# Optimization experiments

Hardware: AMD Instinct MI355X
Metric: run time of the kernel (lower is better)

The kernel has to match this reference:

```python
import jax, jax.numpy as jnp
import numpy as np
from jax import lax

T, B = 80, 32
ACT, CIN, HID, LSTM_H = 16, 4, 512, 256

def _conv(x, w, b, stride, pad):
    y = lax.conv_general_dilated(x, w, (stride, stride), [(pad, pad), (pad, pad)],
                                 dimension_numbers=('NCHW', 'OIHW', 'NCHW'))
    return y + b[None, :, None, None]

def setup_inputs() -> dict:
    key = jax.random.key(0)
    ks = jax.random.split(key, 20)
    s = 0.02
    return {
        'x': jax.random.uniform(ks[0], (T, B, CIN, 84, 84), dtype=jnp.float32),
        'last_action': jax.random.randint(ks[1], (T, B), 0, ACT),
        'reward': jax.random.normal(ks[2], (T, B), dtype=jnp.float32),
        'dones': jnp.zeros((T, B), dtype=bool),
        'hx': jax.random.normal(ks[3], (2, B, LSTM_H), dtype=jnp.float32) * s,
        'conv1_w': jax.random.normal(ks[4], (32, CIN, 8, 8), jnp.float32) * s,
        'conv1_b': jnp.zeros((32,), jnp.float32),
        'conv2_w': jax.random.normal(ks[5], (64, 32, 4, 4), jnp.float32) * s,
        'conv2_b': jnp.zeros((64,), jnp.float32),
        'conv3_w': jax.random.normal(ks[6], (64, 64, 3, 3), jnp.float32) * s,
        'conv3_b': jnp.zeros((64,), jnp.float32),
        'fc_w': jax.random.normal(ks[7], (HID, 3136), jnp.float32) * s,
        'fc_b': jnp.zeros((HID,), jnp.float32),
        'lstm_wih': jax.random.normal(ks[8], (4 * LSTM_H, HID + ACT + 1), jnp.float32) * s,
        'lstm_whh': jax.random.normal(ks[9], (4 * LSTM_H, LSTM_H), jnp.float32) * s,
        'lstm_bih': jnp.zeros((4 * LSTM_H,), jnp.float32),
        'lstm_bhh': jnp.zeros((4 * LSTM_H,), jnp.float32),
        'actor_w': jax.random.normal(ks[10], (ACT, LSTM_H), jnp.float32) * s,
        'actor_b': jnp.zeros((ACT,), jnp.float32),
        'critic_w': jax.random.normal(ks[11], (1, LSTM_H), jnp.float32) * s,
        'critic_b': jnp.zeros((1,), jnp.float32),
    }

def reference(x, last_action, reward, dones, hx,
              conv1_w, conv1_b, conv2_w, conv2_b, conv3_w, conv3_b,
              fc_w, fc_b, lstm_wih, lstm_whh, lstm_bih, lstm_bhh,
              actor_w, actor_b, critic_w, critic_b):
    seq_len, bs = x.shape[0], x.shape[1]
    xf = x.reshape(seq_len * bs, CIN, 84, 84)          # combine time & batch
    la = jax.nn.one_hot(last_action.reshape(-1), ACT, dtype=jnp.float32)
    rw = reward.reshape(-1, 1)

    lrelu = lambda v: jax.nn.leaky_relu(v, 0.01)
    h = lrelu(_conv(xf, conv1_w, conv1_b, 4, 1))       # [N,32,20,20]
    h = lrelu(_conv(h, conv2_w, conv2_b, 2, 0))        # [N,64,9,9]
    h = lrelu(_conv(h, conv3_w, conv3_b, 1, 0))        # [N,64,7,7]
    h = h.reshape(h.shape[0], -1)                      # [N,3136]
    h = lrelu(h @ fc_w.T + fc_b)                       # [N,512]
    h = jnp.concatenate([h, rw, la], axis=1)           # [N,529]
    h = h.reshape(seq_len, bs, -1)

    def step(carry, inp):
        xt, dt = inp                                   # [bs,529], [bs] bool
        carry = jnp.where(dt[None, :, None], 0.0, carry)
        hh, cc = carry[0], carry[1]
        gates = xt @ lstm_wih.T + lstm_bih + hh @ lstm_whh.T + lstm_bhh
        i, f, g, o = jnp.split(gates, 4, axis=1)
        cc = jax.nn.sigmoid(f) * cc + jax.nn.sigmoid(i) * jnp.tanh(g)
        hh = jax.nn.sigmoid(o) * jnp.tanh(cc)
        return jnp.stack([hh, cc], 0), hh

    _, hs = lax.scan(step, hx, (h, dones))             # hs: [T,bs,256]
    feat = hs.reshape(seq_len * bs, LSTM_H)

    logits = feat @ actor_w.T + actor_b                # [N,16]
    values = feat @ critic_w.T + critic_b              # [N,1]
    logits = jnp.where(jnp.isnan(logits), jnp.float32(1e-12), logits)
    return logits.reshape(seq_len, -1, bs), values.reshape(seq_len, bs)
```

## Files before the change

### kernel.cpp

```cpp
#include <hip/hip_runtime.h>
#include <math.h>

#define T_ 80
#define B_ 32
#define N_ 2560
#define LH_ 256

typedef __attribute__((ext_vector_type(8))) short short8;
typedef __attribute__((ext_vector_type(4))) float f32x4;
#define MFMA16(a, b, c) __builtin_amdgcn_mfma_f32_16x16x32_bf16((a), (b), (c), 0, 0, 0)

__device__ __forceinline__ float lrelu(float v) { return v > 0.f ? v : 0.01f * v; }
__device__ __forceinline__ short f2bf(float f) {
    unsigned u = __float_as_uint(f);
    return (short)((u + 0x7fffu + ((u >> 16) & 1u)) >> 16);
}

__global__ void pack_all_k(const float* __restrict__ c1w, const float* __restrict__ c2w,
                           const float* __restrict__ c3w, const float* __restrict__ fcw,
                           const float* __restrict__ wih,
                           short* __restrict__ wp1, short* __restrict__ wp2,
                           short* __restrict__ wp3, short* __restrict__ wfcP,
                           short* __restrict__ wihP) {
    __shared__ short rowb[3136];
    int blk = blockIdx.x, tidx = threadIdx.x;
    if (blk < 512) {
        int j = blk;
        for (int i = tidx; i < 3136; i += 256) rowb[i] = f2bf(fcw[j * 3136 + i]);
        __syncthreads();
        for (int i = tidx; i < 3136; i += 256) {
            int p = i >> 6, oc = i & 63;
            wfcP[j * 3136 + i] = rowb[oc * 49 + p];
        }
        return;
    }
    blk -= 512;
    if (blk < 2048) {
        int g = blk * 256 + tidx;
        int r = g >> 9, k = g & 511;
        wihP[g] = f2bf(wih[r * 529 + k]);
        return;
    }
    blk -= 2048;
    if (blk < 32) {
        int g = blk * 256 + tidx;
        int ky = g >> 10, oc = (g >> 5) & 31, k = g & 31, kx = k >> 2, ci = k & 3;
        wp1[g] = f2bf(c1w[((oc * 4 + ci) * 8 + ky) * 8 + kx]);
        return;
    }
    blk -= 32;
    if (blk < 128) {
        int g = blk * 256 + tidx;
        int t = g >> 11, oc = (g >> 5) & 63, ci = g & 31, ky = t >> 2, kx = t & 3;
        wp2[g] = f2bf(c2w[((oc * 32 + ci) * 4 + ky) * 4 + kx]);
        return;
    }
    blk -= 128;
    {
        int g = blk * 256 + tidx;
        int tkc = g >> 11, oc = (g >> 5) & 63, c32 = g & 31;
        int t = tkc >> 1, kc = tkc & 1, ky = t / 3, kx = t % 3;
        wp3[g] = f2bf(c3w[((oc * 64 + kc * 32 + c32) * 3 + ky) * 3 + kx]);
    }
}

#define C1_RS 344
__global__ __launch_bounds__(512) void conv123_mfma(
    const float* __restrict__ x,
    const short* __restrict__ wp1, const float* __restrict__ b1v,
    const short* __restrict__ wp2, const float* __restrict__ b2v,
    const short* __restrict__ wp3, const float* __restrict__ b3v,
    short* __restrict__ h3) {
    __shared__ short xs[44 * C1_RS];
    __shared__ short h1s[400 * 40];
    __shared__ short ob2[96 * 72];
    int n = blockIdx.x, tid = threadIdx.x;
    int lane = tid & 63, wid = tid >> 6;
    int lr = lane & 15, kq = lane >> 4;

    short8 bfr1[8][2];
#pragma unroll
    for (int ky = 0; ky < 8; ++ky)
#pragma unroll
        for (int nt = 0; nt < 2; ++nt)
            bfr1[ky][nt] = *(const short8*)&wp1[((ky * 32) + nt * 16 + lr) * 32 + kq * 8];
    float b0 = b1v[lr], b1 = b1v[16 + lr];

#pragma unroll
    for (int pass = 0; pass < 2; ++pass) {
        const int iybase = pass ? 39 : -1;
        for (int i = tid; i < 44 * 84; i += 512) {
            int ry = i / 84, xi4 = i % 84;
            int ci = xi4 / 21, x4 = xi4 % 21;
            int iy = iybase + ry;
            if (iy < 0) continue;
            float4 v = *(const float4*)(x + (size_t)(n * 4 + ci) * 7056 + iy * 84 + x4 * 4);
            int base = ry * C1_RS + (x4 * 4 + 1) * 4 + ci;
            xs[base] = f2bf(v.x); xs[base + 4] = f2bf(v.y);
            xs[base + 8] = f2bf(v.z); xs[base + 12] = f2bf(v.w);
        }
        for (int i = tid; i < 44 * 4; i += 512)
            xs[(i >> 2) * C1_RS + (i & 3)] = 0;
        if (pass == 0)
            for (int i = tid; i < C1_RS; i += 512) xs[i] = 0;
        __syncthreads();

        for (int t = wid; t < 13; t += 8) {
            int pl = t * 16 + lr; if (pl > 199) pl = 199;
            int p = pass * 200 + pl;
            int oy = p / 20, ox = p % 20;
            f32x4 acc0 = {0.f, 0.f, 0.f, 0.f}, acc1 = {0.f, 0.f, 0.f, 0.f};
#pragma unroll
            for (int ky = 0; ky < 8; ++ky) {
                int ry = oy * 4 + ky - (pass ? 40 : 0);
                short8 af = *(const short8*)&xs[ry * C1_RS + ox * 16 + kq * 8];
                acc0 = MFMA16(af, bfr1[ky][0], acc0);
                acc1 = MFMA16(af, bfr1[ky][1], acc1);
            }
#pragma unroll
            for (int r = 0; r < 4; ++r) {
                int rp = t * 16 + kq * 4 + r;
                if (rp < 200) {
                    int row = pass * 200 + rp;
                    h1s[row * 40 + lr]      = f2bf(lrelu(acc0[r] + b0));
                    h1s[row * 40 + 16 + lr] = f2bf(lrelu(acc1[r] + b1));
                }
            }
        }
        __syncthreads();
    }

    int nt = wid & 3, mh = wid >> 2;
    {
        short8 bfr[16];
#pragma unroll
        for (int t = 0; t < 16; ++t)
            bfr[t] = *(const short8*)&wp2[(t * 64 + nt * 16 + lr) * 32 + kq * 8];
        float bl = b2v[nt * 16 + lr];
        for (int mt = mh * 3; mt < mh * 3 + 3; ++mt) {
            int p = mt * 16 + lr; if (p > 80) p = 80;
            int oy = p / 9, ox = p % 9;
            f32x4 acc = {0.f, 0.f, 0.f, 0.f};
#pragma unroll
            for (int ky = 0; ky < 4; ++ky)
#pragma unroll
                for (int kx = 0; kx < 4; ++kx) {
                    int pix = (oy * 2 + ky) * 20 + ox * 2 + kx;
                    short8 af = *(const short8*)&h1s[pix * 40 + kq * 8];
                    acc = MFMA16(af, bfr[ky * 4 + kx], acc);
                }
            int pm = mt * 16 + kq * 4;
#pragma unroll
            for (int r = 0; r < 4; ++r)
                ob2[(pm + r) * 72 + nt * 16 + lr] = f2bf(lrelu(acc[r] + bl));
        }
    }
    __syncthreads();
    {
        short8 cfr[18];
#pragma unroll
        for (int t = 0; t < 18; ++t)
            cfr[t] = *(const short8*)&wp3[(t * 64 + nt * 16 + lr) * 32 + kq * 8];
        float bl3 = b3v[nt * 16 + lr];
        short* ob3 = xs;
        for (int mt = mh * 2; mt < mh * 2 + 2; ++mt) {
            int p = mt * 16 + lr; if (p > 48) p = 48;
            int oy = p / 7, ox = p % 7;
            f32x4 acc = {0.f, 0.f, 0.f, 0.f};
#pragma unroll
            for (int ky = 0; ky < 3; ++ky)
#pragma unroll
                for (int kx = 0; kx < 3; ++kx) {
                    int pix = (oy + ky) * 9 + ox + kx;
#pragma unroll
                    for (int kc = 0; kc < 2; ++kc) {
                        short8 af = *(const short8*)&ob2[pix * 72 + kc * 32 + kq * 8];
                        acc = MFMA16(af, cfr[(ky * 3 + kx) * 2 + kc], acc);
                    }
                }
            int pm = mt * 16 + kq * 4;
#pragma unroll
            for (int r = 0; r < 4; ++r)
                ob3[(pm + r) * 64 + nt * 16 + lr] = f2bf(lrelu(acc[r] + bl3));
        }
    }
    __syncthreads();
    uint4* dst = (uint4*)(h3 + (size_t)n * 3136);
    for (int i = tid; i < 392; i += 512) dst[i] = ((uint4*)xs)[i];
}

template <int OUT>
__global__ __launch_bounds__(256) void gemm_bf16(
    const short* __restrict__ A, const short* __restrict__ B,
    const float* __restrict__ bias, void* __restrict__ Cout,
    int M, int N, int K, int ldc,
    const float* __restrict__ reward = nullptr, const int* __restrict__ la = nullptr,
    const float* __restrict__ wih = nullptr, const float* __restrict__ bih = nullptr,
    const float* __restrict__ bhh = nullptr) {
    __shared__ short smem[15360];
    int m0 = blockIdx.y * 128, n0 = blockIdx.x * 64;
    int tid = threadIdx.x;
    int lane = tid & 63, wid = tid >> 6;
    int wr = wid >> 1, wc = wid & 1;
    int lr = lane & 15, kq = lane >> 4;
    f32x4 acc[4][2];
#pragma unroll
    for (int i = 0; i < 4; ++i)
#pragma unroll
        for (int j = 0; j < 2; ++j) acc[i][j] = (f32x4){0.f, 0.f, 0.f, 0.f};

    int nsteps = K >> 5;
#define STAGE(k0, buf)                                                          \
    {                                                                           \
        short* As = smem + (buf) * 5120;                                        \
        short* Bs = smem + 10240 + (buf) * 2560;                                \
        for (int i = tid; i < 512; i += 256) {                                  \
            int row = i >> 2, c4 = i & 3;                                       \
            *(uint4*)&As[row * 40 + c4 * 8] =                                   \
                *(const uint4*)&A[(size_t)(m0 + row) * K + (k0) + c4 * 8];      \
        }                                                                       \
        {                                                                       \
            int row = tid >> 2, c4 = tid & 3;                                   \
            *(uint4*)&Bs[row * 40 + c4 * 8] =                                   \
                *(const uint4*)&B[(size_t)(n0 + row) * K + (k0) + c4 * 8];      \
        }                                                                       \
    }
    STAGE(0, 0);
    __syncthreads();
    for (int ks = 0; ks < nsteps; ++ks) {
        int buf = ks & 1;
        if (ks + 1 < nsteps) STAGE((ks + 1) * 32, buf ^ 1);
        short* As = smem + buf * 5120;
        short* Bs = smem + 10240 + buf * 2560;
        short8 af[4], bfr[2];
#pragma unroll
        for (int i = 0; i < 4; ++i)
            af[i] = *(const short8*)&As[(wr * 64 + i * 16 + lr) * 40 + kq * 8];
#pragma unroll
        for (int j = 0; j < 2; ++j)
            bfr[j] = *(const short8*)&Bs[(wc * 32 + j * 16 + lr) * 40 + kq * 8];
#pragma unroll
        for (int i = 0; i < 4; ++i)
#pragma unroll
            for (int j = 0; j < 2; ++j)
                acc[i][j] = MFMA16(af[i], bfr[j], acc[i][j]);
        __syncthreads();
    }
#undef STAGE
    if (OUT == 2) {
        float* C = (float*)Cout;
#pragma unroll
        for (int i = 0; i < 4; ++i)
#pragma unroll
            for (int j = 0; j < 2; ++j) {
                int col = n0 + wc * 32 + j * 16 + lr;
                const float* wrow = wih + (size_t)col * 529;
                float base = bih[col] + bhh[col];
                float w512 = wrow[512];
#pragma unroll
                for (int r = 0; r < 4; ++r) {
                    int row = m0 + wr * 64 + i * 16 + kq * 4 + r;
                    C[(size_t)row * ldc + col] =
                        acc[i][j][r] + base + reward[row] * w512 + wrow[513 + la[row]];
                }
            }
    } else {
        short* ob = smem;
#pragma unroll
        for (int i = 0; i < 4; ++i)
#pragma unroll
            for (int j = 0; j < 2; ++j) {
                int col = wc * 32 + j * 16 + lr;
                float bl = bias[n0 + col];
#pragma unroll
                for (int r = 0; r < 4; ++r) {
                    int row = wr * 64 + i * 16 + kq * 4 + r;
                    ob[row * 64 + col] = f2bf(lrelu(acc[i][j][r] + bl));
                }
            }
        __syncthreads();
        short* C = (short*)Cout;
        for (int i = tid; i < 1024; i += 256) {
            int row = i >> 3, c8 = i & 7;
            *(uint4*)&C[(size_t)(m0 + row) * ldc + n0 + c8 * 8] =
                *(uint4*)&ob[row * 64 + c8 * 8];
        }
    }
}

__global__ __launch_bounds__(512, 2) void lstm_bs_k(
    const float* __restrict__ gx,
    const float* __restrict__ whh,
    const unsigned char* __restrict__ dones,
    const float* __restrict__ hx,
    float* __restrict__ hs) {
    const int tid = threadIdx.x;
    const int g2 = blockIdx.x;
    const int lane = tid & 63, w = tid >> 6;
    const int lr = lane & 15, kq = lane >> 4;

    __shared__ short wL[65536];
    __shared__ short hB[16 * 264];
    __shared__ float gate_s[4 * 256 * 2];

    short8 afr[6][8];
#pragma unroll
    for (int mi = 0; mi < 6; ++mi) {
        int row = w * 128 + mi * 16 + lr;
        const float* wrp = whh + (size_t)row * 256;
#pragma unroll
        for (int kt = 0; kt < 8; ++kt) {
            int k0 = kt * 32 + kq * 8;
            float4 a = *(const float4*)(wrp + k0);
            float4 b = *(const float4*)(wrp + k0 + 4);
            short8 f;
            f[0] = f2bf(a.x); f[1] = f2bf(a.y); f[2] = f2bf(a.z); f[3] = f2bf(a.w);
            f[4] = f2bf(b.x); f[5] = f2bf(b.y); f[6] = f2bf(b.z); f[7] = f2bf(b.w);
            afr[mi][kt] = f;
        }
    }
    {
        int* ap = (int*)afr;
#pragma unroll
        for (int i = 0; i < 192; ++i) asm volatile("" : "+v"(ap[i]));
    }

    for (int s = tid; s < 8192; s += 512) {
        int w2 = s >> 10, m2 = (s >> 9) & 1, kt = (s >> 6) & 7, ln = s & 63;
        int row = w2 * 128 + (6 + m2) * 16 + (ln & 15);
        int k0 = kt * 32 + (ln >> 4) * 8;
        const float* wrp = whh + (size_t)row * 256 + k0;
        short8 f;
#pragma unroll
        for (int e = 0; e < 8; ++e) f[e] = f2bf(wrp[e]);
        *(short8*)&wL[s * 8] = f;
    }

    for (int i = tid; i < 14 * 264; i += 512) hB[2 * 264 + i] = 0;

    const int u = tid >> 1, bt = tid & 1;
    const int b = g2 * 2 + bt;
    float cc = hx[(size_t)B_ * LH_ + b * LH_ + u];

    {
        int bt2 = tid >> 8, k = tid & 255;
        int b2 = g2 * 2 + bt2;
        float hv = hx[b2 * LH_ + k];
        if (dones[b2]) hv = 0.f;
        hB[bt2 * 264 + k] = f2bf(hv);
    }
    __syncthreads();

    for (int t = 1; t <= T_; ++t) {
        const int nb0 = (t - 1) * B_;
        float gxv[4];
#pragma unroll
        for (int gg2 = 0; gg2 < 4; ++gg2)
            gxv[gg2] = gx[(size_t)(nb0 + b) * 1024 + gg2 * 256 + u];

        f32x4 acc[8];
#pragma unroll
        for (int mi = 0; mi < 8; ++mi) acc[mi] = (f32x4){0.f, 0.f, 0.f, 0.f};
#pragma unroll
        for (int kt = 0; kt < 8; ++kt) {
            short8 bfr = *(const short8*)&hB[lr * 264 + kt * 32 + kq * 8];
#pragma unroll
            for (int mi = 0; mi < 6; ++mi)
                acc[mi] = MFMA16(afr[mi][kt], bfr, acc[mi]);
#pragma unroll
            for (int m2 = 0; m2 < 2; ++m2) {
                short8 lA = *(const short8*)&wL[(((w * 2 + m2) * 8 + kt) * 64 + lane) * 8];
                acc[6 + m2] = MFMA16(lA, bfr, acc[6 + m2]);
            }
        }
        if (lr < 2) {
#pragma unroll
            for (int mi = 0; mi < 8; ++mi)
#pragma unroll
                for (int r = 0; r < 4; ++r) {
                    int row = w * 128 + mi * 16 + kq * 4 + r;
                    gate_s[(row >> 8) * 512 + (row & 255) * 2 + lr] = acc[mi][r];
                }
        }
        __syncthreads();

        {
            bool dn = dones[nb0 + b] != 0;
            float gi = gate_s[0 * 512 + u * 2 + bt] + gxv[0];
            float gf = gate_s[1 * 512 + u * 2 + bt] + gxv[1];
            float gg = gate_s[2 * 512 + u * 2 + bt] + gxv[2];
            float go = gate_s[3 * 512 + u * 2 + bt] + gxv[3];
            float ccv = dn ? 0.f : cc;
            float si = 1.f / (1.f + expf(-gi));
            float sf = 1.f / (1.f + expf(-gf));
            float so = 1.f / (1.f + expf(-go));
            float c2 = sf * ccv + si * tanhf(gg);
            float h2 = so * tanhf(c2);
            cc = c2;
            if (t < T_) {
                hB[bt * 264 + u] = f2bf(dones[t * B_ + b] ? 0.f : h2);
            }
            hs[(size_t)(nb0 + b) * LH_ + u] = h2;
        }
        __syncthreads();
    }
}

__global__ void head_k(const float* __restrict__ hs,
                       const float* __restrict__ aw, const float* __restrict__ ab,
                       const float* __restrict__ cw, const float* __restrict__ cb,
                       float* __restrict__ out) {
    int gid = blockIdx.x * 256 + threadIdx.x;
    if (gid >= N_ * 17) return;
    int n = gid / 17, r = gid % 17;
    const float* f = hs + (size_t)n * 256;
    if (r < 16) {
        const float* w = aw + r * 256;
        float acc = ab[r];
        for (int k = 0; k < 256; ++k) acc = fmaf(f[k], w[k], acc);
        if (isnan(acc)) acc = 1e-12f;
        out[(size_t)n * 16 + r] = acc;
    } else {
        float acc = cb[0];
        for (int k = 0; k < 256; ++k) acc = fmaf(f[k], cw[k], acc);
        out[(size_t)N_ * 16 + n] = acc;
    }
}

extern "C" void kernel_launch(void* const* d_in, const int* in_sizes, int n_in,
                              void* d_out, int out_size, void* d_ws, size_t ws_size,
                              hipStream_t stream) {
    const float* x      = (const float*)d_in[0];
    const int* la       = (const int*)d_in[1];
    const float* reward = (const float*)d_in[2];
    const unsigned char* dones = (const unsigned char*)d_in[3];
    const float* hx     = (const float*)d_in[4];
    const float* c1w = (const float*)d_in[5];  const float* c1b = (const float*)d_in[6];
    const float* c2w = (const float*)d_in[7];  const float* c2b = (const float*)d_in[8];
    const float* c3w = (const float*)d_in[9];  const float* c3b = (const float*)d_in[10];
    const float* fcw = (const float*)d_in[11]; const float* fcb = (const float*)d_in[12];
    const float* wih = (const float*)d_in[13]; const float* whh = (const float*)d_in[14];
    const float* bih = (const float*)d_in[15]; const float* bhh = (const float*)d_in[16];
    const float* aw  = (const float*)d_in[17]; const float* ab  = (const float*)d_in[18];
    const float* cw  = (const float*)d_in[19]; const float* cb  = (const float*)d_in[20];

    char* wsb = (char*)d_ws;
    short* h3   = (short*)(wsb + 92078080);
    short* hfc  = (short*)(wsb + 108134400);
    float* gx   = (float*)(wsb + 110755840);
    float* hs   = (float*)(wsb + 121241600);
    short* wp1  = (short*)(wsb + 123932672);
    short* wp2  = (short*)(wsb + 123949056);
    short* wp3  = (short*)(wsb + 124014592);
    short* wfcP = (short*)(wsb + 124088320);
    short* wihP = (short*)(wsb + 127299584);

    pack_all_k<<<2864, 256, 0, stream>>>(c1w, c2w, c3w, fcw, wih,
                                         wp1, wp2, wp3, wfcP, wihP);

    conv123_mfma<<<2560, 512, 0, stream>>>(x, wp1, c1b, wp2, c2b, wp3, c3b, h3);

    gemm_bf16<1><<<dim3(8, 20), 256, 0, stream>>>(h3, wfcP, fcb, hfc,
                                                  2560, 512, 3136, 512);
    gemm_bf16<2><<<dim3(16, 20), 256, 0, stream>>>(hfc, wihP, nullptr, gx,
                                                   2560, 1024, 512, 1024,
                                                   reward, la, wih, bih, bhh);

    lstm_bs_k<<<16, 512, 0, stream>>>(gx, whh, dones, hx, hs);
    head_k<<<170, 256, 0, stream>>>(hs, aw, ab, cw, cb, (float*)d_out);
}
```

Measured before the change: 468.1 us.

## Prefetch next-step gate inputs, split LSTM MFMA accumulators, fuse head into LSTM kernel

The LSTM recurrence now loads the next timestep's input-gate values while the current step's MFMA work runs, which takes global-load latency off the serial critical path. The recurrent matmul is split into two passes of four accumulators to lower register pressure. The actor/critic head kernel is removed and its work runs at the end of the LSTM kernel, saving one launch. The cost is that the head now runs on only 16 blocks instead of 170, which may make it slower.

```diff
diff --git a/kernel.cpp b/kernel.cpp
--- a/kernel.cpp
+++ b/kernel.cpp
@@ -293,7 +293,10 @@
     const float* __restrict__ whh,
     const unsigned char* __restrict__ dones,
     const float* __restrict__ hx,
-    float* __restrict__ hs) {
+    float* __restrict__ hs,
+    const float* __restrict__ aw, const float* __restrict__ ab,
+    const float* __restrict__ cw, const float* __restrict__ cb,
+    float* __restrict__ outp) {
     const int tid = threadIdx.x;
     const int g2 = blockIdx.x;
     const int lane = tid & 63, w = tid >> 6;
@@ -349,38 +352,66 @@
         if (dones[b2]) hv = 0.f;
         hB[bt2 * 264 + k] = f2bf(hv);
     }
+    float gxv[4];
+#pragma unroll
+    for (int gg2 = 0; gg2 < 4; ++gg2)
+        gxv[gg2] = gx[(size_t)b * 1024 + gg2 * 256 + u];
     __syncthreads();
 
     for (int t = 1; t <= T_; ++t) {
         const int nb0 = (t - 1) * B_;
-        float gxv[4];
-#pragma unroll
-        for (int gg2 = 0; gg2 < 4; ++gg2)
-            gxv[gg2] = gx[(size_t)(nb0 + b) * 1024 + gg2 * 256 + u];
-
-        f32x4 acc[8];
-#pragma unroll
-        for (int mi = 0; mi < 8; ++mi) acc[mi] = (f32x4){0.f, 0.f, 0.f, 0.f};
-#pragma unroll
-        for (int kt = 0; kt < 8; ++kt) {
-            short8 bfr = *(const short8*)&hB[lr * 264 + kt * 32 + kq * 8];
-#pragma unroll
-            for (int mi = 0; mi < 6; ++mi)
-                acc[mi] = MFMA16(afr[mi][kt], bfr, acc[mi]);
-#pragma unroll
-            for (int m2 = 0; m2 < 2; ++m2) {
-                short8 lA = *(const short8*)&wL[(((w * 2 + m2) * 8 + kt) * 64 + lane) * 8];
-                acc[6 + m2] = MFMA16(lA, bfr, acc[6 + m2]);
-            }
-        }
-        if (lr < 2) {
-#pragma unroll
-            for (int mi = 0; mi < 8; ++mi)
-#pragma unroll
-                for (int r = 0; r < 4; ++r) {
-                    int row = w * 128 + mi * 16 + kq * 4 + r;
-                    gate_s[(row >> 8) * 512 + (row & 255) * 2 + lr] = acc[mi][r];
+        float gxn[4];
+        if (t < T_) {
+#pragma unroll
+            for (int gg2 = 0; gg2 < 4; ++gg2)
+                gxn[gg2] = gx[(size_t)(t * B_ + b) * 1024 + gg2 * 256 + u];
+        }
+
+        {
+            f32x4 acc[4];
+#pragma unroll
+            for (int mi = 0; mi < 4; ++mi) acc[mi] = (f32x4){0.f, 0.f, 0.f, 0.f};
+#pragma unroll
+            for (int kt = 0; kt < 8; ++kt) {
+                short8 bfr = *(const short8*)&hB[lr * 264 + kt * 32 + kq * 8];
+#pragma unroll
+                for (int mi = 0; mi < 4; ++mi)
+                    acc[mi] = MFMA16(afr[mi][kt], bfr, acc[mi]);
+            }
+            if (lr < 2) {
+#pragma unroll
+                for (int mi = 0; mi < 4; ++mi)
+#pragma unroll
+                    for (int r = 0; r < 4; ++r) {
+                        int row = w * 128 + mi * 16 + kq * 4 + r;
+                        gate_s[(row >> 8) * 512 + (row & 255) * 2 + lr] = acc[mi][r];
+                    }
+            }
+        }
+        {
+            f32x4 acc[4];
+#pragma unroll
+            for (int mi = 0; mi < 4; ++mi) acc[mi] = (f32x4){0.f, 0.f, 0.f, 0.f};
+#pragma unroll
+            for (int kt = 0; kt < 8; ++kt) {
+                short8 bfr = *(const short8*)&hB[lr * 264 + kt * 32 + kq * 8];
+                acc[0] = MFMA16(afr[4][kt], bfr, acc[0]);
+                acc[1] = MFMA16(afr[5][kt], bfr, acc[1]);
+#pragma unroll
+                for (int m2 = 0; m2 < 2; ++m2) {
+                    short8 lA = *(const short8*)&wL[(((w * 2 + m2) * 8 + kt) * 64 + lane) * 8];
+                    acc[2 + m2] = MFMA16(lA, bfr, acc[2 + m2]);
                 }
+            }
+            if (lr < 2) {
+#pragma unroll
+                for (int mi = 0; mi < 4; ++mi)
+#pragma unroll
+                    for (int r = 0; r < 4; ++r) {
+                        int row = w * 128 + (4 + mi) * 16 + kq * 4 + r;
+                        gate_s[(row >> 8) * 512 + (row & 255) * 2 + lr] = acc[mi][r];
+                    }
+            }
         }
         __syncthreads();
 
@@ -402,28 +433,27 @@
             }
             hs[(size_t)(nb0 + b) * LH_ + u] = h2;
         }
-        __syncthreads();
-    }
-}
-
-__global__ void head_k(const float* __restrict__ hs,
-                       const float* __restrict__ aw, const float* __restrict__ ab,
-                       const float* __restrict__ cw, const float* __restrict__ cb,
-                       float* __restrict__ out) {
-    int gid = blockIdx.x * 256 + threadIdx.x;
-    if (gid >= N_ * 17) return;
-    int n = gid / 17, r = gid % 17;
-    const float* f = hs + (size_t)n * 256;
-    if (r < 16) {
-        const float* w = aw + r * 256;
-        float acc = ab[r];
-        for (int k = 0; k < 256; ++k) acc = fmaf(f[k], w[k], acc);
-        if (isnan(acc)) acc = 1e-12f;
-        out[(size_t)n * 16 + r] = acc;
-    } else {
-        float acc = cb[0];
-        for (int k = 0; k < 256; ++k) acc = fmaf(f[k], cw[k], acc);
-        out[(size_t)N_ * 16 + n] = acc;
+#pragma unroll
+        for (int gg2 = 0; gg2 < 4; ++gg2) gxv[gg2] = gxn[gg2];
+        __syncthreads();
+    }
+
+    for (int i = tid; i < 2720; i += 512) {
+        int r17 = i % 17, tb = i / 17;
+        int t = tb >> 1, bt2 = tb & 1;
+        int n = t * B_ + g2 * 2 + bt2;
+        const float* f = hs + (size_t)n * LH_;
+        if (r17 < 16) {
+            const float* wv = aw + r17 * 256;
+            float a2 = ab[r17];
+            for (int k = 0; k < 256; ++k) a2 = fmaf(f[k], wv[k], a2);
+            if (isnan(a2)) a2 = 1e-12f;
+            outp[(size_t)n * 16 + r17] = a2;
+        } else {
+            float a2 = cb[0];
+            for (int k = 0; k < 256; ++k) a2 = fmaf(f[k], cw[k], a2);
+            outp[(size_t)N_ * 16 + n] = a2;
+        }
     }
 }
 
@@ -466,6 +496,6 @@
                                                    2560, 1024, 512, 1024,
                                                    reward, la, wih, bih, bhh);
 
-    lstm_bs_k<<<16, 512, 0, stream>>>(gx, whh, dones, hx, hs);
-    head_k<<<170, 256, 0, stream>>>(hs, aw, ab, cw, cb, (float*)d_out);
+    lstm_bs_k<<<16, 512, 0, stream>>>(gx, whh, dones, hx, hs,
+                                      aw, ab, cw, cb, (float*)d_out);
 }
```

Measured after the change: 632.5 us. +35.1%, slower.
